# Kernel tuning notes

Hardware: AMD Instinct MI355X
Metric: run time of the kernel (lower is better)

Reference implementation:

```python
import jax, jax.numpy as jnp
import numpy as np

N = 65536   # number of latents in the bank
D = 1024    # latent dimensionality
NEIGHBORS = 64  # cfg.system.loss.latent_manifold_neighbors


def setup_inputs() -> dict:
    key = jax.random.key(0)
    all_latents = jax.random.normal(key, (N, D), dtype=jnp.float32)
    group_id = 123  # scalar index into the latent bank
    return {"group_id": group_id, "all_latents": all_latents}


def reference(group_id, all_latents):
    # selected_latents: [D]
    sel = all_latents[group_id]
    # diff: [N, D]; torch.norm(diff, p=2, dim=0) reduces over the sample axis N -> [D]
    dist = jnp.sqrt(jnp.sum((sel[None, :] - all_latents) ** 2, axis=0))
    # k smallest per-feature distances (topk largest=False)
    dist_small = -jax.lax.top_k(-dist, NEIGHBORS)[0]
    return dist_small.mean()
```

## Files before the change

kernel.cpp:

```cpp
#include <hip/hip_runtime.h>

#define N_ROWS  65536
#define D       1024
#define NB      512
#define TPB     256
#define RPT     (N_ROWS / NB)
#define K_NEIGH 64

__global__ __launch_bounds__(TPB) void lm_colsumsq(
    const int* __restrict__ gid,
    const float* __restrict__ x,
    float* __restrict__ acc)
{
    const int t   = threadIdx.x;
    const int col = t << 2;
    const int g   = gid[0];

    const float4 sel = *reinterpret_cast<const float4*>(x + (size_t)g * D + col);

    float a0 = 0.f, a1 = 0.f, a2 = 0.f, a3 = 0.f;
    const float* p = x + (size_t)blockIdx.x * D + col;

    #pragma unroll 8
    for (int i = 0; i < RPT; ++i) {
        float4 v = *reinterpret_cast<const float4*>(p);
        p += (size_t)NB * D;
        float d0 = sel.x - v.x;
        float d1 = sel.y - v.y;
        float d2 = sel.z - v.z;
        float d3 = sel.w - v.w;
        a0 = fmaf(d0, d0, a0);
        a1 = fmaf(d1, d1, a1);
        a2 = fmaf(d2, d2, a2);
        a3 = fmaf(d3, d3, a3);
    }

    atomicAdd(&acc[col + 0], a0);
    atomicAdd(&acc[col + 1], a1);
    atomicAdd(&acc[col + 2], a2);
    atomicAdd(&acc[col + 3], a3);
}

__global__ __launch_bounds__(D) void lm_topk(
    const float* __restrict__ acc,
    float* __restrict__ out)
{
    __shared__ float s[D];
    const int d = threadIdx.x;

    s[d] = acc[d];
    __syncthreads();

    for (int k = 2; k <= D; k <<= 1) {
        for (int j = k >> 1; j > 0; j >>= 1) {
            int ixj = d ^ j;
            if (ixj > d) {
                float a = s[d], b = s[ixj];
                bool asc = ((d & k) == 0);
                if ((a > b) == asc) { s[d] = b; s[ixj] = a; }
            }
            __syncthreads();
        }
    }

    if (d < K_NEIGH) {
        float v = sqrtf(s[d]);
        #pragma unroll
        for (int off = 32; off > 0; off >>= 1) v += __shfl_down(v, off);
        if (d == 0) out[0] = v * (1.0f / K_NEIGH);
    }
}

extern "C" void kernel_launch(void* const* d_in, const int* in_sizes, int n_in,
                              void* d_out, int out_size, void* d_ws, size_t ws_size,
                              hipStream_t stream)
{
    const int*   gid = (const int*)d_in[0];
    const float* x   = (const float*)d_in[1];
    float*       out = (float*)d_out;
    float*       acc = (float*)d_ws;

    hipMemsetAsync(acc, 0, D * sizeof(float), stream);

    lm_colsumsq<<<NB, TPB, 0, stream>>>(gid, x, acc);
    lm_topk<<<1, D, 0, stream>>>(acc, out);
}
```

Measured before the change: 394.0 us.

## Fuse top-k into column reduction via last-block pattern and spread atomics

Merges the column sum-of-squares kernel and the bitonic top-k kernel into one launch. The last block to finish, found through an atomic counter, sums the partial accumulators and sorts. Atomics are also spread over 8 accumulator copies to reduce contention on the same addresses. This removes one kernel launch and its gap, but the final sort now runs on 256 threads instead of 1024 and adds threadfence overhead.

```diff
diff --git a/kernel.cpp b/kernel.cpp
--- a/kernel.cpp
+++ b/kernel.cpp
@@ -6,11 +6,13 @@
 #define TPB     256
 #define RPT     (N_ROWS / NB)
 #define K_NEIGH 64
+#define NACC    8
 
-__global__ __launch_bounds__(TPB) void lm_colsumsq(
+__global__ __launch_bounds__(TPB) void lm_fused(
     const int* __restrict__ gid,
     const float* __restrict__ x,
-    float* __restrict__ acc)
+    float* __restrict__ ws,
+    float* __restrict__ out)
 {
     const int t   = threadIdx.x;
     const int col = t << 2;
@@ -35,39 +37,53 @@
         a3 = fmaf(d3, d3, a3);
     }
 
+    float* acc = ws + (size_t)(blockIdx.x & (NACC - 1)) * D;
     atomicAdd(&acc[col + 0], a0);
     atomicAdd(&acc[col + 1], a1);
     atomicAdd(&acc[col + 2], a2);
     atomicAdd(&acc[col + 3], a3);
-}
 
-__global__ __launch_bounds__(D) void lm_topk(
-    const float* __restrict__ acc,
-    float* __restrict__ out)
-{
+    __shared__ int is_last;
+    __threadfence();
+    if (t == 0) {
+        unsigned* cnt = (unsigned*)(ws + NACC * D);
+        unsigned old = atomicAdd(cnt, 1u);
+        is_last = (old == NB - 1);
+    }
+    __syncthreads();
+    if (!is_last) return;
+
+    __threadfence();
     __shared__ float s[D];
-    const int d = threadIdx.x;
-
-    s[d] = acc[d];
+    for (int c = t; c < D; c += TPB) {
+        float v = 0.f;
+        #pragma unroll
+        for (int r = 0; r < NACC; ++r)
+            v += __hip_atomic_load(&ws[(size_t)r * D + c],
+                                   __ATOMIC_RELAXED, __HIP_MEMORY_SCOPE_AGENT);
+        s[c] = v;
+    }
     __syncthreads();
 
     for (int k = 2; k <= D; k <<= 1) {
         for (int j = k >> 1; j > 0; j >>= 1) {
-            int ixj = d ^ j;
-            if (ixj > d) {
-                float a = s[d], b = s[ixj];
-                bool asc = ((d & k) == 0);
-                if ((a > b) == asc) { s[d] = b; s[ixj] = a; }
+            for (int dd = t; dd < D; dd += TPB) {
+                int ixj = dd ^ j;
+                if (ixj > dd) {
+                    float a = s[dd], b = s[ixj];
+                    bool asc = ((dd & k) == 0);
+                    if ((a > b) == asc) { s[dd] = b; s[ixj] = a; }
+                }
             }
             __syncthreads();
         }
     }
 
-    if (d < K_NEIGH) {
-        float v = sqrtf(s[d]);
+    if (t < K_NEIGH) {
+        float v = sqrtf(s[t]);
         #pragma unroll
         for (int off = 32; off > 0; off >>= 1) v += __shfl_down(v, off);
-        if (d == 0) out[0] = v * (1.0f / K_NEIGH);
+        if (t == 0) out[0] = v * (1.0f / K_NEIGH);
     }
 }
 
@@ -78,10 +94,9 @@
     const int*   gid = (const int*)d_in[0];
     const float* x   = (const float*)d_in[1];
     float*       out = (float*)d_out;
-    float*       acc = (float*)d_ws;
+    float*       ws  = (float*)d_ws;
 
-    hipMemsetAsync(acc, 0, D * sizeof(float), stream);
+    hipMemsetAsync(ws, 0, (NACC * D) * sizeof(float) + sizeof(unsigned), stream);
 
-    lm_colsumsq<<<NB, TPB, 0, stream>>>(gid, x, acc);
-    lm_topk<<<1, D, 0, stream>>>(acc, out);
+    lm_fused<<<NB, TPB, 0, stream>>>(gid, x, ws, out);
 }
```

Result: slower. 455.2 us (+15.5%).
